# Kernel optimization log

Hardware: AMD Instinct MI355X
Metric: run time of the kernel (lower is better)

## Reference

```python
import jax, jax.numpy as jnp
import numpy as np

D = 128          # fine voxel grid resolution
N0 = 250000
D_IN, D_BASE, D_OUT = 16, 8, 8
EPS = 1e-5
# (cin, cout) for conv0..conv6, conv7, conv9, conv11
_CH = [(16, 8), (8, 16), (16, 16), (16, 32), (32, 32), (32, 64), (64, 64), (64, 32), (32, 16), (16, 8)]

def _offsets():
    r = np.arange(-1, 2)
    return np.stack(np.meshgrid(r, r, r, indexing='ij'), -1).reshape(-1, 3)  # [27,3]

def _lookup_fn(coords, d):
    keys = (coords[:, 0].astype(np.int64) * d + coords[:, 1]) * d + coords[:, 2]
    order = np.argsort(keys)
    skeys = keys[order]
    def lookup(q):
        valid = ((q >= 0) & (q < d)).all(-1)
        k = (q[:, 0].astype(np.int64) * d + q[:, 1]) * d + q[:, 2]
        pos = np.clip(np.searchsorted(skeys, k), 0, len(skeys) - 1)
        return np.where(valid & (skeys[pos] == k), order[pos], -1).astype(np.int32)
    return lookup

def _nbr_same(coords, d):
    # stride-1 sparse conv: outputs at input coords, neighbors at coord+k
    lk = _lookup_fn(coords, d)
    return np.stack([lk(coords + o) for o in _offsets()], 1)  # [N,27]

def _nbr_down(c_out, c_in, d_in):
    # stride-2 conv: output p gathers inputs at 2p+k
    lk = _lookup_fn(c_in, d_in)
    return np.stack([lk(c_out * 2 + o) for o in _offsets()], 1)

def _nbr_up(c_out, c_in, d_in):
    # transposed stride-2 conv: output q gathers input p=(q-k)/2 where divisible
    lk = _lookup_fn(c_in, d_in)
    cols = []
    for o in _offsets():
        q = c_out - o
        div = (q % 2 == 0).all(-1)
        cols.append(np.where(div, lk(q // 2), -1).astype(np.int32))
    return np.stack(cols, 1)

def setup_inputs():
    rng = np.random.default_rng(0)
    flat = rng.choice(D ** 3, size=N0, replace=False)
    c0 = np.stack([flat // (D * D), (flat // D) % D, flat % D], 1).astype(np.int32)
    c1 = np.unique(c0 // 2, axis=0)
    c2 = np.unique(c1 // 2, axis=0)
    c3 = np.unique(c2 // 2, axis=0)
    inp = {
        'feats': jax.random.normal(jax.random.key(0), (N0, D_IN), jnp.float32),
        'nbr0': jnp.asarray(_nbr_same(c0, D)),
        'nbr_d01': jnp.asarray(_nbr_down(c1, c0, D)),
        'nbr1': jnp.asarray(_nbr_same(c1, D // 2)),
        'nbr_d12': jnp.asarray(_nbr_down(c2, c1, D // 2)),
        'nbr2': jnp.asarray(_nbr_same(c2, D // 4)),
        'nbr_d23': jnp.asarray(_nbr_down(c3, c2, D // 4)),
        'nbr3': jnp.asarray(_nbr_same(c3, D // 8)),
        'nbr_u32': jnp.asarray(_nbr_up(c2, c3, D // 8)),
        'nbr_u21': jnp.asarray(_nbr_up(c1, c2, D // 4)),
        'nbr_u10': jnp.asarray(_nbr_up(c0, c1, D // 2)),
    }
    key = jax.random.key(1)
    for i, (ci, co) in enumerate(_CH):
        key, kw = jax.random.split(key)
        inp['w%d' % i] = jax.random.normal(kw, (27, ci, co), jnp.float32) / np.sqrt(27.0 * ci)
        inp['g%d' % i] = jnp.ones((co,), jnp.float32)
        inp['b%d' % i] = jnp.zeros((co,), jnp.float32)
    inp['lin_w'] = jax.random.normal(jax.random.key(2), (D_OUT, D_BASE), jnp.float32) / np.sqrt(D_BASE)
    return inp

def _sconv_bn_relu(f, nbr, w, g, b):
    # f: [Nin,Cin], nbr: [Nout,27] (-1 = no neighbor), w: [27,Cin,Cout]
    gth = jnp.where((nbr >= 0)[..., None], f[jnp.maximum(nbr, 0)], 0.0)  # [Nout,27,Cin]
    y = jnp.einsum('nkc,kco->no', gth, w)
    mu = y.mean(0)                       # training-mode BatchNorm over active voxels
    var = y.var(0)
    return jax.nn.relu((y - mu) * jax.lax.rsqrt(var + EPS) * g + b)

def reference(feats, nbr0, nbr_d01, nbr1, nbr_d12, nbr2, nbr_d23, nbr3, nbr_u32, nbr_u21, nbr_u10,
              w0, g0, b0, w1, g1, b1, w2, g2, b2, w3, g3, b3, w4, g4, b4,
              w5, g5, b5, w6, g6, b6, w7, g7, b7, w8, g8, b8, w9, g9, b9, lin_w):
    c0f = _sconv_bn_relu(feats, nbr0, w0, g0, b0)
    c2f = _sconv_bn_relu(_sconv_bn_relu(c0f, nbr_d01, w1, g1, b1), nbr1, w2, g2, b2)
    c4f = _sconv_bn_relu(_sconv_bn_relu(c2f, nbr_d12, w3, g3, b3), nbr2, w4, g4, b4)
    x = _sconv_bn_relu(_sconv_bn_relu(c4f, nbr_d23, w5, g5, b5), nbr3, w6, g6, b6)
    x = c4f + _sconv_bn_relu(x, nbr_u32, w7, g7, b7)
    x = c2f + _sconv_bn_relu(x, nbr_u21, w8, g8, b8)
    x = c0f + _sconv_bn_relu(x, nbr_u10, w9, g9, b9)
    return x @ lin_w.T, x
```

## Files before the change

kernel.cpp:

```cpp
#include <hip/hip_runtime.h>

#define EPSV 1e-5f

typedef __attribute__((ext_vector_type(8))) short short8;
typedef __attribute__((ext_vector_type(4))) float float4v;

static inline int cdiv(int a, int b) { return (a + b - 1) / b; }

__device__ inline unsigned short f2bf(float x) {
  unsigned u = __float_as_uint(x);
  return (unsigned short)((u + 0x7FFFu + ((u >> 16) & 1u)) >> 16);
}
__device__ inline float bf2f(unsigned short u) {
  return __uint_as_float(((unsigned)u) << 16);
}

#define NBUCKET 64

struct PrepArgs {
  const float* w[10];
  unsigned short* wt[10];
  int ci[10];
  int co[10];
  int wcum[11];
  const float* feats;
  unsigned short* featsb;
  int nfeat4;
  float* stats;
};

__global__ __launch_bounds__(256) void prep_kernel(PrepArgs p) {
  long tid = (long)blockIdx.x * 256 + threadIdx.x;
  const int nstat4 = 10 * NBUCKET * 128 / 4;
  if (tid < nstat4) {
    ((float4*)p.stats)[tid] = make_float4(0.f, 0.f, 0.f, 0.f);
    return;
  }
  tid -= nstat4;
  if (tid < p.nfeat4) {
    float4 v = ((const float4*)p.feats)[tid];
    ushort4 r;
    r.x = f2bf(v.x); r.y = f2bf(v.y); r.z = f2bf(v.z); r.w = f2bf(v.w);
    ((ushort4*)p.featsb)[tid] = r;
    return;
  }
  tid -= p.nfeat4;
  if (tid >= p.wcum[10]) return;
  int i = 0;
  while (tid >= p.wcum[i + 1]) ++i;
  int e = (int)(tid - p.wcum[i]);
  int ci = p.ci[i], co = p.co[i];
  int k = e / (ci * co);
  int r = e - k * (ci * co);
  int o = r / ci;
  int c = r - o * ci;
  p.wt[i][((long)k * co + o) * ci + c] = f2bf(p.w[i][((long)k * ci + c) * co + o]);
}

template<int CI, int CO>
__global__ __launch_bounds__(256) void conv_mfma(
    const unsigned short* __restrict__ f, const int* __restrict__ nbr,
    const unsigned short* __restrict__ wt, unsigned short* __restrict__ y,
    float* __restrict__ stats, int nout, int nxb) {
  constexpr int NCHUNK = (CI == 8) ? 7 : (CI == 16) ? 14 : (CI == 32) ? 27 : 54;

  int bx = blockIdx.x, xb;
  {
    int S8 = nxb >> 3;
    if (bx < (S8 << 3)) xb = (bx & 7) * S8 + (bx >> 3);
    else xb = bx;
  }

  const int tid = threadIdx.x;
  const int lane = tid & 63;
  const int wid = tid >> 6;
  const int m = lane & 15;
  const int quad = lane >> 4;
  const int blockrow = xb * 64;
  const int row = blockrow + wid * 16 + m;
  const bool rok = row < nout;
  const int cbase = blockIdx.y * 16;
  const int co = cbase + m;
  const bool cok = co < CO;

  auto tapof = [&](int c) -> int {
    if constexpr (CI == 8) return c * 4 + quad;
    else if constexpr (CI == 16) return c * 2 + (quad >> 1);
    else if constexpr (CI == 32) return c;
    else return c >> 1;
  };
  auto cioof = [&](int c) -> int {
    if constexpr (CI == 8) return 0;
    else if constexpr (CI == 16) return (quad & 1) * 8;
    else if constexpr (CI == 32) return quad * 8;
    else return ((c & 1) << 5) + quad * 8;
  };

  float4v acc = {0.f, 0.f, 0.f, 0.f};

  if constexpr (CI <= 16) {
    int idxs[NCHUNK];
#pragma unroll
    for (int c = 0; c < NCHUNK; ++c) {
      int tap = tapof(c);
      idxs[c] = (rok && tap < 27) ? nbr[(long)row * 27 + tap] : -1;
    }
    short8 A[NCHUNK], B[NCHUNK];
#pragma unroll
    for (int c = 0; c < NCHUNK; ++c) {
      int tap = tapof(c);
      short8 a, bq;
#pragma unroll
      for (int q = 0; q < 8; ++q) { a[q] = 0; bq[q] = 0; }
      if (idxs[c] >= 0) a = *(const short8*)(f + (long)idxs[c] * CI + cioof(c));
      if (cok && tap < 27) bq = *(const short8*)(wt + ((long)tap * CO + co) * CI + cioof(c));
      A[c] = a; B[c] = bq;
    }
#pragma unroll
    for (int c = 0; c < NCHUNK; ++c)
      acc = __builtin_amdgcn_mfma_f32_16x16x32_bf16(A[c], B[c], acc, 0, 0, 0);
  } else {
    constexpr int G = 9;
    constexpr int NG = NCHUNK / G;
    int idxs[27];
#pragma unroll
    for (int t = 0; t < 27; ++t)
      idxs[t] = rok ? nbr[(long)row * 27 + t] : -1;

    short8 A[2][G], B[2][G];
    auto load_group = [&](int g, int bi) {
#pragma unroll
      for (int j = 0; j < G; ++j) {
        const int c = g * G + j;
        const int tap = tapof(c);
        short8 a, bq;
#pragma unroll
        for (int q = 0; q < 8; ++q) { a[q] = 0; bq[q] = 0; }
        int idx = idxs[tap];
        if (idx >= 0) a = *(const short8*)(f + (long)idx * CI + cioof(c));
        if (cok) bq = *(const short8*)(wt + ((long)tap * CO + co) * CI + cioof(c));
        A[bi][j] = a; B[bi][j] = bq;
      }
    };
    load_group(0, 0);
#pragma unroll
    for (int g = 0; g < NG; ++g) {
      const int cur = g & 1;
      if (g + 1 < NG) load_group(g + 1, cur ^ 1);
#pragma unroll
      for (int j = 0; j < G; ++j)
        acc = __builtin_amdgcn_mfma_f32_16x16x32_bf16(A[cur][j], B[cur][j], acc, 0, 0, 0);
    }
  }

  float sum = 0.f, sq = 0.f;
#pragma unroll
  for (int r = 0; r < 4; ++r) {
    float v = acc[r];
    int orow = blockrow + wid * 16 + quad * 4 + r;
    if (cok && orow < nout) y[(long)orow * CO + co] = f2bf(v);
    sum += v;
    sq = fmaf(v, v, sq);
  }
  sum += __shfl_xor(sum, 16); sq += __shfl_xor(sq, 16);
  sum += __shfl_xor(sum, 32); sq += __shfl_xor(sq, 32);
  if (quad == 0 && cok) {
    float* st = stats + (((unsigned)xb & (NBUCKET - 1)) << 7);
    atomicAdd(&st[co], sum);
    atomicAdd(&st[64 + co], sq);
  }
}

template<int CO>
__global__ __launch_bounds__(256) void bn_relu_bf16(
    const unsigned short* __restrict__ y, const float* __restrict__ stats,
    const float* __restrict__ g, const float* __restrict__ b,
    const unsigned short* __restrict__ skip, unsigned short* __restrict__ out,
    int nout, float inv_n) {
  __shared__ float sA[CO], sC[CO];
  if ((int)threadIdx.x < CO) {
    int o = threadIdx.x;
    float su = 0.f, sq = 0.f;
#pragma unroll 8
    for (int bk = 0; bk < NBUCKET; ++bk) {
      su += stats[bk * 128 + o];
      sq += stats[bk * 128 + 64 + o];
    }
    float mu = su * inv_n;
    float var = sq * inv_n - mu * mu;
    float a = g[o] * rsqrtf(var + EPSV);
    sA[o] = a;
    sC[o] = fmaf(-mu, a, b[o]);
  }
  __syncthreads();
  long i4 = (long)blockIdx.x * 256 + threadIdx.x;
  long total4 = (long)nout * CO / 4;
  if (i4 >= total4) return;
  int o = (int)((i4 * 4) % CO);
  ushort4 v = ((const ushort4*)y)[i4];
  float vv[4] = {bf2f(v.x), bf2f(v.y), bf2f(v.z), bf2f(v.w)};
  unsigned short rr[4];
#pragma unroll
  for (int j = 0; j < 4; ++j) {
    float x = fmaxf(fmaf(vv[j], sA[o + j], sC[o + j]), 0.f);
    if (skip) x += bf2f(skip[i4 * 4 + j]);
    rr[j] = f2bf(x);
  }
  ushort4 r;
  r.x = rr[0]; r.y = rr[1]; r.z = rr[2]; r.w = rr[3];
  ((ushort4*)out)[i4] = r;
}

__global__ __launch_bounds__(256) void tail_kernel(
    const unsigned short* __restrict__ c0f, const float* __restrict__ st9,
    const float* __restrict__ g9, const float* __restrict__ b9, float inv_n,
    const float* __restrict__ lin_w, const unsigned short* __restrict__ y9,
    float* __restrict__ out0, float* __restrict__ x0, int n0) {
  __shared__ float swl[64];
  __shared__ float sbn[16];
  if (threadIdx.x < 64) swl[threadIdx.x] = lin_w[threadIdx.x];
  if (threadIdx.x < 8) {
    int o = threadIdx.x;
    float su = 0.f, sq = 0.f;
#pragma unroll 8
    for (int bk = 0; bk < NBUCKET; ++bk) {
      su += st9[bk * 128 + o];
      sq += st9[bk * 128 + 64 + o];
    }
    float mu = su * inv_n;
    float var = sq * inv_n - mu * mu;
    float a = g9[o] * rsqrtf(var + EPSV);
    sbn[o] = a;
    sbn[8 + o] = fmaf(-mu, a, b9[o]);
  }
  __syncthreads();
  int n = blockIdx.x * 256 + threadIdx.x;
  if (n >= n0) return;
  const ushort4* pr = (const ushort4*)(y9 + (long)n * 8);
  ushort4 r0 = pr[0], r1 = pr[1];
  unsigned short rw[8] = {r0.x, r0.y, r0.z, r0.w, r1.x, r1.y, r1.z, r1.w};
  const ushort4* pc = (const ushort4*)(c0f + (long)n * 8);
  ushort4 c0 = pc[0], c1 = pc[1];
  unsigned short cs[8] = {c0.x, c0.y, c0.z, c0.w, c1.x, c1.y, c1.z, c1.w};
  float xv[8];
#pragma unroll
  for (int c = 0; c < 8; ++c)
    xv[c] = bf2f(cs[c]) + fmaxf(fmaf(bf2f(rw[c]), sbn[c], sbn[8 + c]), 0.f);
  *(float4*)(x0 + (long)n * 8) = make_float4(xv[0], xv[1], xv[2], xv[3]);
  *(float4*)(x0 + (long)n * 8 + 4) = make_float4(xv[4], xv[5], xv[6], xv[7]);
  float ov[8];
#pragma unroll
  for (int j = 0; j < 8; ++j) {
    float s = 0.f;
#pragma unroll
    for (int c = 0; c < 8; ++c) s = fmaf(xv[c], swl[j * 8 + c], s);
    ov[j] = s;
  }
  *(float4*)(out0 + (long)n * 8) = make_float4(ov[0], ov[1], ov[2], ov[3]);
  *(float4*)(out0 + (long)n * 8 + 4) = make_float4(ov[4], ov[5], ov[6], ov[7]);
}

extern "C" void kernel_launch(void* const* d_in, const int* in_sizes, int n_in,
                              void* d_out, int out_size, void* d_ws, size_t ws_size,
                              hipStream_t stream) {
  const float* feats   = (const float*)d_in[0];
  const int* nbr0      = (const int*)d_in[1];
  const int* nbr_d01   = (const int*)d_in[2];
  const int* nbr1      = (const int*)d_in[3];
  const int* nbr_d12   = (const int*)d_in[4];
  const int* nbr2      = (const int*)d_in[5];
  const int* nbr_d23   = (const int*)d_in[6];
  const int* nbr3      = (const int*)d_in[7];
  const int* nbr_u32   = (const int*)d_in[8];
  const int* nbr_u21   = (const int*)d_in[9];
  const int* nbr_u10   = (const int*)d_in[10];
  const float* w[10];
  const float* g[10];
  const float* b[10];
  for (int i = 0; i < 10; ++i) {
    w[i] = (const float*)d_in[11 + 3 * i];
    g[i] = (const float*)d_in[12 + 3 * i];
    b[i] = (const float*)d_in[13 + 3 * i];
  }
  const float* lin_w = (const float*)d_in[41];

  const int N0 = in_sizes[0] / 16;
  const int N1 = in_sizes[2] / 27;
  const int N2 = in_sizes[4] / 27;
  const int N3 = in_sizes[6] / 27;
  const float i0 = 1.f / N0, i1 = 1.f / N1, i2 = 1.f / N2, i3 = 1.f / N3;

  static const int CIv[10] = {16, 8, 16, 16, 32, 32, 64, 64, 32, 16};
  static const int COv[10] = {8, 16, 16, 32, 32, 64, 64, 32, 16, 8};

  float* stats = (float*)d_ws;
  unsigned short* u = (unsigned short*)(stats + 10 * NBUCKET * 128);

  unsigned short* yraw = u; u += (size_t)N1 * 32;

  unsigned short* wt[10];
  int wcum[11];
  wcum[0] = 0;
  for (int i = 0; i < 10; ++i) {
    wt[i] = u;
    int sz = 27 * CIv[i] * COv[i];
    u += sz;
    wcum[i + 1] = wcum[i] + sz;
  }
  unsigned short* featsb = u; u += (size_t)N0 * 16;
  unsigned short* c0f = u;    u += (size_t)N0 * 8;
  unsigned short* t1  = u;    u += (size_t)N1 * 16;
  unsigned short* c2f = u;    u += (size_t)N1 * 16;
  unsigned short* t2  = u;    u += (size_t)N2 * 32;
  unsigned short* c4f = u;    u += (size_t)N2 * 32;
  unsigned short* t3  = u;    u += (size_t)N3 * 64;
  unsigned short* t4  = u;    u += (size_t)N3 * 64;
  unsigned short* t5  = t2;
  unsigned short* t6  = t1;
  float* out0 = (float*)d_out;
  float* x0   = (float*)d_out + (size_t)N0 * 8;

  float* s[10];
  for (int i = 0; i < 10; ++i) s[i] = stats + i * NBUCKET * 128;

  PrepArgs pa;
  for (int i = 0; i < 10; ++i) {
    pa.w[i] = w[i]; pa.wt[i] = wt[i];
    pa.ci[i] = CIv[i]; pa.co[i] = COv[i];
    pa.wcum[i] = wcum[i];
  }
  pa.wcum[10] = wcum[10];
  pa.feats = feats; pa.featsb = featsb;
  pa.nfeat4 = N0 * 16 / 4;
  pa.stats = stats;
  long prep_total = (10 * NBUCKET * 128 / 4) + pa.nfeat4 + wcum[10];
  prep_kernel<<<(int)((prep_total + 255) / 256), 256, 0, stream>>>(pa);

  auto bgrid = [](long nout, int co) { return (int)((nout * co / 4 + 255) / 256); };

  int xb0 = cdiv(N0, 64), xb1 = cdiv(N1, 64), xb2 = cdiv(N2, 64), xb3 = cdiv(N3, 64);

  conv_mfma<16, 8><<<dim3(xb0, 1), 256, 0, stream>>>(featsb, nbr0, wt[0], yraw, s[0], N0, xb0);
  bn_relu_bf16<8><<<bgrid(N0, 8), 256, 0, stream>>>(yraw, s[0], g[0], b[0], nullptr, c0f, N0, i0);

  conv_mfma<8, 16><<<dim3(xb1, 1), 256, 0, stream>>>(c0f, nbr_d01, wt[1], yraw, s[1], N1, xb1);
  bn_relu_bf16<16><<<bgrid(N1, 16), 256, 0, stream>>>(yraw, s[1], g[1], b[1], nullptr, t1, N1, i1);

  conv_mfma<16, 16><<<dim3(xb1, 1), 256, 0, stream>>>(t1, nbr1, wt[2], yraw, s[2], N1, xb1);
  bn_relu_bf16<16><<<bgrid(N1, 16), 256, 0, stream>>>(yraw, s[2], g[2], b[2], nullptr, c2f, N1, i1);

  conv_mfma<16, 32><<<dim3(xb2, 2), 256, 0, stream>>>(c2f, nbr_d12, wt[3], yraw, s[3], N2, xb2);
  bn_relu_bf16<32><<<bgrid(N2, 32), 256, 0, stream>>>(yraw, s[3], g[3], b[3], nullptr, t2, N2, i2);

  conv_mfma<32, 32><<<dim3(xb2, 2), 256, 0, stream>>>(t2, nbr2, wt[4], yraw, s[4], N2, xb2);
  bn_relu_bf16<32><<<bgrid(N2, 32), 256, 0, stream>>>(yraw, s[4], g[4], b[4], nullptr, c4f, N2, i2);

  conv_mfma<32, 64><<<dim3(xb3, 4), 256, 0, stream>>>(c4f, nbr_d23, wt[5], yraw, s[5], N3, xb3);
  bn_relu_bf16<64><<<bgrid(N3, 64), 256, 0, stream>>>(yraw, s[5], g[5], b[5], nullptr, t3, N3, i3);

  conv_mfma<64, 64><<<dim3(xb3, 4), 256, 0, stream>>>(t3, nbr3, wt[6], yraw, s[6], N3, xb3);
  bn_relu_bf16<64><<<bgrid(N3, 64), 256, 0, stream>>>(yraw, s[6], g[6], b[6], nullptr, t4, N3, i3);

  conv_mfma<64, 32><<<dim3(xb2, 2), 256, 0, stream>>>(t4, nbr_u32, wt[7], yraw, s[7], N2, xb2);
  bn_relu_bf16<32><<<bgrid(N2, 32), 256, 0, stream>>>(yraw, s[7], g[7], b[7], c4f, t5, N2, i2);

  conv_mfma<32, 16><<<dim3(xb1, 1), 256, 0, stream>>>(t5, nbr_u21, wt[8], yraw, s[8], N1, xb1);
  bn_relu_bf16<16><<<bgrid(N1, 16), 256, 0, stream>>>(yraw, s[8], g[8], b[8], c2f, t6, N1, i1);

  conv_mfma<16, 8><<<dim3(xb0, 1), 256, 0, stream>>>(t6, nbr_u10, wt[9], yraw, s[9], N0, xb0);

  tail_kernel<<<cdiv(N0, 256), 256, 0, stream>>>(c0f, s[9], g[9], b[9], i0, lin_w, yraw, out0, x0, N0);
}
```

Baseline: 501.8 us.

## Convert conv and elementwise kernels to grid-stride persistent loops

Every kernel (prep, conv, BN-ReLU, tail) now runs a grid-stride loop, with grids capped at 1024 or 2048 blocks. For the small-CI convs the weight fragments are loaded once per block and reused across tiles, and BN stat partial sums accumulate in registers across tiles, so fewer atomics are issued. The XCD-aware block swizzle is dropped, and stat buckets are now keyed by block and wave. The cost is less latency hiding from oversubscription and possible load imbalance, since consecutive tiles no longer map to the same XCD.

New measurement: 480.0 us. 1.05x faster.

```diff
diff --git a/kernel.cpp b/kernel.cpp
--- a/kernel.cpp
+++ b/kernel.cpp
@@ -6,6 +6,7 @@
 typedef __attribute__((ext_vector_type(4))) float float4v;
 
 static inline int cdiv(int a, int b) { return (a + b - 1) / b; }
+static inline int imin(int a, int b) { return a < b ? a : b; }
 
 __device__ inline unsigned short f2bf(float x) {
   unsigned u = __float_as_uint(x);
@@ -29,56 +30,49 @@
   float* stats;
 };
 
-__global__ __launch_bounds__(256) void prep_kernel(PrepArgs p) {
-  long tid = (long)blockIdx.x * 256 + threadIdx.x;
+__global__ __launch_bounds__(256) void prep_kernel(PrepArgs p, long total) {
   const int nstat4 = 10 * NBUCKET * 128 / 4;
-  if (tid < nstat4) {
-    ((float4*)p.stats)[tid] = make_float4(0.f, 0.f, 0.f, 0.f);
-    return;
-  }
-  tid -= nstat4;
-  if (tid < p.nfeat4) {
-    float4 v = ((const float4*)p.feats)[tid];
-    ushort4 r;
-    r.x = f2bf(v.x); r.y = f2bf(v.y); r.z = f2bf(v.z); r.w = f2bf(v.w);
-    ((ushort4*)p.featsb)[tid] = r;
-    return;
-  }
-  tid -= p.nfeat4;
-  if (tid >= p.wcum[10]) return;
-  int i = 0;
-  while (tid >= p.wcum[i + 1]) ++i;
-  int e = (int)(tid - p.wcum[i]);
-  int ci = p.ci[i], co = p.co[i];
-  int k = e / (ci * co);
-  int r = e - k * (ci * co);
-  int o = r / ci;
-  int c = r - o * ci;
-  p.wt[i][((long)k * co + o) * ci + c] = f2bf(p.w[i][((long)k * ci + c) * co + o]);
+  for (long tid0 = (long)blockIdx.x * 256 + threadIdx.x; tid0 < total;
+       tid0 += (long)gridDim.x * 256) {
+    long tid = tid0;
+    if (tid < nstat4) {
+      ((float4*)p.stats)[tid] = make_float4(0.f, 0.f, 0.f, 0.f);
+      continue;
+    }
+    tid -= nstat4;
+    if (tid < p.nfeat4) {
+      float4 v = ((const float4*)p.feats)[tid];
+      ushort4 r;
+      r.x = f2bf(v.x); r.y = f2bf(v.y); r.z = f2bf(v.z); r.w = f2bf(v.w);
+      ((ushort4*)p.featsb)[tid] = r;
+      continue;
+    }
+    tid -= p.nfeat4;
+    if (tid >= p.wcum[10]) continue;
+    int i = 0;
+    while (tid >= p.wcum[i + 1]) ++i;
+    int e = (int)(tid - p.wcum[i]);
+    int ci = p.ci[i], co = p.co[i];
+    int k = e / (ci * co);
+    int r = e - k * (ci * co);
+    int o = r / ci;
+    int c = r - o * ci;
+    p.wt[i][((long)k * co + o) * ci + c] = f2bf(p.w[i][((long)k * ci + c) * co + o]);
+  }
 }
 
 template<int CI, int CO>
 __global__ __launch_bounds__(256) void conv_mfma(
     const unsigned short* __restrict__ f, const int* __restrict__ nbr,
     const unsigned short* __restrict__ wt, unsigned short* __restrict__ y,
-    float* __restrict__ stats, int nout, int nxb) {
+    float* __restrict__ stats, int nout, int ntiles) {
   constexpr int NCHUNK = (CI == 8) ? 7 : (CI == 16) ? 14 : (CI == 32) ? 27 : 54;
-
-  int bx = blockIdx.x, xb;
-  {
-    int S8 = nxb >> 3;
-    if (bx < (S8 << 3)) xb = (bx & 7) * S8 + (bx >> 3);
-    else xb = bx;
-  }
 
   const int tid = threadIdx.x;
   const int lane = tid & 63;
   const int wid = tid >> 6;
   const int m = lane & 15;
   const int quad = lane >> 4;
-  const int blockrow = xb * 64;
-  const int row = blockrow + wid * 16 + m;
-  const bool rok = row < nout;
   const int cbase = blockIdx.y * 16;
   const int co = cbase + m;
   const bool cok = co < CO;
@@ -96,76 +90,103 @@
     else return ((c & 1) << 5) + quad * 8;
   };
 
-  float4v acc = {0.f, 0.f, 0.f, 0.f};
+  float sum = 0.f, sq = 0.f;
 
   if constexpr (CI <= 16) {
-    int idxs[NCHUNK];
+    short8 Bv[NCHUNK];
 #pragma unroll
     for (int c = 0; c < NCHUNK; ++c) {
       int tap = tapof(c);
-      idxs[c] = (rok && tap < 27) ? nbr[(long)row * 27 + tap] : -1;
-    }
-    short8 A[NCHUNK], B[NCHUNK];
-#pragma unroll
-    for (int c = 0; c < NCHUNK; ++c) {
-      int tap = tapof(c);
-      short8 a, bq;
-#pragma unroll
-      for (int q = 0; q < 8; ++q) { a[q] = 0; bq[q] = 0; }
-      if (idxs[c] >= 0) a = *(const short8*)(f + (long)idxs[c] * CI + cioof(c));
+      short8 bq;
+#pragma unroll
+      for (int q = 0; q < 8; ++q) bq[q] = 0;
       if (cok && tap < 27) bq = *(const short8*)(wt + ((long)tap * CO + co) * CI + cioof(c));
-      A[c] = a; B[c] = bq;
-    }
-#pragma unroll
-    for (int c = 0; c < NCHUNK; ++c)
-      acc = __builtin_amdgcn_mfma_f32_16x16x32_bf16(A[c], B[c], acc, 0, 0, 0);
+      Bv[c] = bq;
+    }
+    for (int tile = blockIdx.x; tile < ntiles; tile += gridDim.x) {
+      const int rowb = tile * 64 + wid * 16;
+      const int row = rowb + m;
+      const bool rok = row < nout;
+      int idxs[NCHUNK];
+#pragma unroll
+      for (int c = 0; c < NCHUNK; ++c) {
+        int tap = tapof(c);
+        idxs[c] = (rok && tap < 27) ? nbr[(long)row * 27 + tap] : -1;
+      }
+      short8 A[NCHUNK];
+#pragma unroll
+      for (int c = 0; c < NCHUNK; ++c) {
+        short8 a;
+#pragma unroll
+        for (int q = 0; q < 8; ++q) a[q] = 0;
+        if (idxs[c] >= 0) a = *(const short8*)(f + (long)idxs[c] * CI + cioof(c));
+        A[c] = a;
+      }
+      float4v acc = {0.f, 0.f, 0.f, 0.f};
+#pragma unroll
+      for (int c = 0; c < NCHUNK; ++c)
+        acc = __builtin_amdgcn_mfma_f32_16x16x32_bf16(A[c], Bv[c], acc, 0, 0, 0);
+#pragma unroll
+      for (int r = 0; r < 4; ++r) {
+        float v = acc[r];
+        int orow = rowb + quad * 4 + r;
+        if (cok && orow < nout) y[(long)orow * CO + co] = f2bf(v);
+        sum += v;
+        sq = fmaf(v, v, sq);
+      }
+    }
   } else {
     constexpr int G = 9;
     constexpr int NG = NCHUNK / G;
-    int idxs[27];
-#pragma unroll
-    for (int t = 0; t < 27; ++t)
-      idxs[t] = rok ? nbr[(long)row * 27 + t] : -1;
-
-    short8 A[2][G], B[2][G];
-    auto load_group = [&](int g, int bi) {
-#pragma unroll
-      for (int j = 0; j < G; ++j) {
-        const int c = g * G + j;
-        const int tap = tapof(c);
-        short8 a, bq;
-#pragma unroll
-        for (int q = 0; q < 8; ++q) { a[q] = 0; bq[q] = 0; }
-        int idx = idxs[tap];
-        if (idx >= 0) a = *(const short8*)(f + (long)idx * CI + cioof(c));
-        if (cok) bq = *(const short8*)(wt + ((long)tap * CO + co) * CI + cioof(c));
-        A[bi][j] = a; B[bi][j] = bq;
-      }
-    };
-    load_group(0, 0);
-#pragma unroll
-    for (int g = 0; g < NG; ++g) {
-      const int cur = g & 1;
-      if (g + 1 < NG) load_group(g + 1, cur ^ 1);
-#pragma unroll
-      for (int j = 0; j < G; ++j)
-        acc = __builtin_amdgcn_mfma_f32_16x16x32_bf16(A[cur][j], B[cur][j], acc, 0, 0, 0);
-    }
-  }
-
-  float sum = 0.f, sq = 0.f;
-#pragma unroll
-  for (int r = 0; r < 4; ++r) {
-    float v = acc[r];
-    int orow = blockrow + wid * 16 + quad * 4 + r;
-    if (cok && orow < nout) y[(long)orow * CO + co] = f2bf(v);
-    sum += v;
-    sq = fmaf(v, v, sq);
-  }
+    for (int tile = blockIdx.x; tile < ntiles; tile += gridDim.x) {
+      const int rowb = tile * 64 + wid * 16;
+      const int row = rowb + m;
+      const bool rok = row < nout;
+      int idxs[27];
+#pragma unroll
+      for (int t = 0; t < 27; ++t)
+        idxs[t] = rok ? nbr[(long)row * 27 + t] : -1;
+
+      short8 A[2][G], B[2][G];
+      auto load_group = [&](int g, int bi) {
+#pragma unroll
+        for (int j = 0; j < G; ++j) {
+          const int c = g * G + j;
+          const int tap = tapof(c);
+          short8 a, bq;
+#pragma unroll
+          for (int q = 0; q < 8; ++q) { a[q] = 0; bq[q] = 0; }
+          int idx = idxs[tap];
+          if (idx >= 0) a = *(const short8*)(f + (long)idx * CI + cioof(c));
+          if (cok) bq = *(const short8*)(wt + ((long)tap * CO + co) * CI + cioof(c));
+          A[bi][j] = a; B[bi][j] = bq;
+        }
+      };
+      float4v acc = {0.f, 0.f, 0.f, 0.f};
+      load_group(0, 0);
+#pragma unroll
+      for (int g = 0; g < NG; ++g) {
+        const int cur = g & 1;
+        if (g + 1 < NG) load_group(g + 1, cur ^ 1);
+#pragma unroll
+        for (int j = 0; j < G; ++j)
+          acc = __builtin_amdgcn_mfma_f32_16x16x32_bf16(A[cur][j], B[cur][j], acc, 0, 0, 0);
+      }
+#pragma unroll
+      for (int r = 0; r < 4; ++r) {
+        float v = acc[r];
+        int orow = rowb + quad * 4 + r;
+        if (cok && orow < nout) y[(long)orow * CO + co] = f2bf(v);
+        sum += v;
+        sq = fmaf(v, v, sq);
+      }
+    }
+  }
+
   sum += __shfl_xor(sum, 16); sq += __shfl_xor(sq, 16);
   sum += __shfl_xor(sum, 32); sq += __shfl_xor(sq, 32);
   if (quad == 0 && cok) {
-    float* st = stats + (((unsigned)xb & (NBUCKET - 1)) << 7);
+    float* st = stats + ((((unsigned)blockIdx.x * 4 + wid) & (NBUCKET - 1)) << 7);
     atomicAdd(&st[co], sum);
     atomicAdd(&st[64 + co], sq);
   }
@@ -193,22 +214,23 @@
     sC[o] = fmaf(-mu, a, b[o]);
   }
   __syncthreads();
-  long i4 = (long)blockIdx.x * 256 + threadIdx.x;
   long total4 = (long)nout * CO / 4;
-  if (i4 >= total4) return;
-  int o = (int)((i4 * 4) % CO);
-  ushort4 v = ((const ushort4*)y)[i4];
-  float vv[4] = {bf2f(v.x), bf2f(v.y), bf2f(v.z), bf2f(v.w)};
-  unsigned short rr[4];
-#pragma unroll
-  for (int j = 0; j < 4; ++j) {
-    float x = fmaxf(fmaf(vv[j], sA[o + j], sC[o + j]), 0.f);
-    if (skip) x += bf2f(skip[i4 * 4 + j]);
-    rr[j] = f2bf(x);
-  }
-  ushort4 r;
-  r.x = rr[0]; r.y = rr[1]; r.z = rr[2]; r.w = rr[3];
-  ((ushort4*)out)[i4] = r;
+  for (long i4 = (long)blockIdx.x * 256 + threadIdx.x; i4 < total4;
+       i4 += (long)gridDim.x * 256) {
+    int o = (int)((i4 * 4) % CO);
+    ushort4 v = ((const ushort4*)y)[i4];
+    float vv[4] = {bf2f(v.x), bf2f(v.y), bf2f(v.z), bf2f(v.w)};
+    unsigned short rr[4];
+#pragma unroll
+    for (int j = 0; j < 4; ++j) {
+      float x = fmaxf(fmaf(vv[j], sA[o + j], sC[o + j]), 0.f);
+      if (skip) x += bf2f(skip[i4 * 4 + j]);
+      rr[j] = f2bf(x);
+    }
+    ushort4 r;
+    r.x = rr[0]; r.y = rr[1]; r.z = rr[2]; r.w = rr[3];
+    ((ushort4*)out)[i4] = r;
+  }
 }
 
 __global__ __launch_bounds__(256) void tail_kernel(
@@ -234,30 +256,30 @@
     sbn[8 + o] = fmaf(-mu, a, b9[o]);
   }
   __syncthreads();
-  int n = blockIdx.x * 256 + threadIdx.x;
-  if (n >= n0) return;
-  const ushort4* pr = (const ushort4*)(y9 + (long)n * 8);
-  ushort4 r0 = pr[0], r1 = pr[1];
-  unsigned short rw[8] = {r0.x, r0.y, r0.z, r0.w, r1.x, r1.y, r1.z, r1.w};
-  const ushort4* pc = (const ushort4*)(c0f + (long)n * 8);
-  ushort4 c0 = pc[0], c1 = pc[1];
-  unsigned short cs[8] = {c0.x, c0.y, c0.z, c0.w, c1.x, c1.y, c1.z, c1.w};
-  float xv[8];
-#pragma unroll
-  for (int c = 0; c < 8; ++c)
-    xv[c] = bf2f(cs[c]) + fmaxf(fmaf(bf2f(rw[c]), sbn[c], sbn[8 + c]), 0.f);
-  *(float4*)(x0 + (long)n * 8) = make_float4(xv[0], xv[1], xv[2], xv[3]);
-  *(float4*)(x0 + (long)n * 8 + 4) = make_float4(xv[4], xv[5], xv[6], xv[7]);
-  float ov[8];
-#pragma unroll
-  for (int j = 0; j < 8; ++j) {
-    float s = 0.f;
-#pragma unroll
-    for (int c = 0; c < 8; ++c) s = fmaf(xv[c], swl[j * 8 + c], s);
-    ov[j] = s;
-  }
-  *(float4*)(out0 + (long)n * 8) = make_float4(ov[0], ov[1], ov[2], ov[3]);
-  *(float4*)(out0 + (long)n * 8 + 4) = make_float4(ov[4], ov[5], ov[6], ov[7]);
+  for (int n = blockIdx.x * 256 + threadIdx.x; n < n0; n += gridDim.x * 256) {
+    const ushort4* pr = (const ushort4*)(y9 + (long)n * 8);
+    ushort4 r0 = pr[0], r1 = pr[1];
+    unsigned short rw[8] = {r0.x, r0.y, r0.z, r0.w, r1.x, r1.y, r1.z, r1.w};
+    const ushort4* pc = (const ushort4*)(c0f + (long)n * 8);
+    ushort4 c0 = pc[0], c1 = pc[1];
+    unsigned short cs[8] = {c0.x, c0.y, c0.z, c0.w, c1.x, c1.y, c1.z, c1.w};
+    float xv[8];
+#pragma unroll
+    for (int c = 0; c < 8; ++c)
+      xv[c] = bf2f(cs[c]) + fmaxf(fmaf(bf2f(rw[c]), sbn[c], sbn[8 + c]), 0.f);
+    *(float4*)(x0 + (long)n * 8) = make_float4(xv[0], xv[1], xv[2], xv[3]);
+    *(float4*)(x0 + (long)n * 8 + 4) = make_float4(xv[4], xv[5], xv[6], xv[7]);
+    float ov[8];
+#pragma unroll
+    for (int j = 0; j < 8; ++j) {
+      float s = 0.f;
+#pragma unroll
+      for (int c = 0; c < 8; ++c) s = fmaf(xv[c], swl[j * 8 + c], s);
+      ov[j] = s;
+    }
+    *(float4*)(out0 + (long)n * 8) = make_float4(ov[0], ov[1], ov[2], ov[3]);
+    *(float4*)(out0 + (long)n * 8 + 4) = make_float4(ov[4], ov[5], ov[6], ov[7]);
+  }
 }
 
 extern "C" void kernel_launch(void* const* d_in, const int* in_sizes, int n_in,
@@ -334,40 +356,44 @@
   pa.nfeat4 = N0 * 16 / 4;
   pa.stats = stats;
   long prep_total = (10 * NBUCKET * 128 / 4) + pa.nfeat4 + wcum[10];
-  prep_kernel<<<(int)((prep_total + 255) / 256), 256, 0, stream>>>(pa);
-
-  auto bgrid = [](long nout, int co) { return (int)((nout * co / 4 + 255) / 256); };
-
-  int xb0 = cdiv(N0, 64), xb1 = cdiv(N1, 64), xb2 = cdiv(N2, 64), xb3 = cdiv(N3, 64);
-
-  conv_mfma<16, 8><<<dim3(xb0, 1), 256, 0, stream>>>(featsb, nbr0, wt[0], yraw, s[0], N0, xb0);
+  prep_kernel<<<imin((int)((prep_total + 255) / 256), 2048), 256, 0, stream>>>(pa, prep_total);
+
+  auto bgrid = [](long nout, int co) {
+    return imin((int)((nout * co / 4 + 255) / 256), 1024);
+  };
+  auto cgrid = [](int ntiles) { return imin(ntiles, 1024); };
+
+  int tb0 = cdiv(N0, 64), tb1 = cdiv(N1, 64), tb2 = cdiv(N2, 64), tb3 = cdiv(N3, 64);
+
+  conv_mfma<16, 8><<<dim3(cgrid(tb0), 1), 256, 0, stream>>>(featsb, nbr0, wt[0], yraw, s[0], N0, tb0);
   bn_relu_bf16<8><<<bgrid(N0, 8), 256, 0, stream>>>(yraw, s[0], g[0], b[0], nullptr, c0f, N0, i0);
 
-  conv_mfma<8, 16><<<dim3(xb1, 1), 256, 0, stream>>>(c0f, nbr_d01, wt[1], yraw, s[1], N1, xb1);
+  conv_mfma<8, 16><<<dim3(cgrid(tb1), 1), 256, 0, stream>>>(c0f, nbr_d01, wt[1], yraw, s[1], N1, tb1);
   bn_relu_bf16<16><<<bgrid(N1, 16), 256, 0, stream>>>(yraw, s[1], g[1], b[1], nullptr, t1, N1, i1);
 
-  conv_mfma<16, 16><<<dim3(xb1, 1), 256, 0, stream>>>(t1, nbr1, wt[2], yraw, s[2], N1, xb1);
+  conv_mfma<16, 16><<<dim3(cgrid(tb1), 1), 256, 0, stream>>>(t1, nbr1, wt[2], yraw, s[2], N1, tb1);
   bn_relu_bf16<16><<<bgrid(N1, 16), 256, 0, stream>>>(yraw, s[2], g[2], b[2], nullptr, c2f, N1, i1);
 
-  conv_mfma<16, 32><<<dim3(xb2, 2), 256, 0, stream>>>(c2f, nbr_d12, wt[3], yraw, s[3], N2, xb2);
+  conv_mfma<16, 32><<<dim3(cgrid(tb2), 2), 256, 0, stream>>>(c2f, nbr_d12, wt[3], yraw, s[3], N2, tb2);
   bn_relu_bf16<32><<<bgrid(N2, 32), 256, 0, stream>>>(yraw, s[3], g[3], b[3], nullptr, t2, N2, i2);
 
-  conv_mfma<32, 32><<<dim3(xb2, 2), 256, 0, stream>>>(t2, nbr2, wt[4], yraw, s[4], N2, xb2);
+  conv_mfma<32, 32><<<dim3(cgrid(tb2), 2), 256, 0, stream>>>(t2, nbr2, wt[4], yraw, s[4], N2, tb2);
   bn_relu_bf16<32><<<bgrid(N2, 32), 256, 0, stream>>>(yraw, s[4], g[4], b[4], nullptr, c4f, N2, i2);
 
-  conv_mfma<32, 64><<<dim3(xb3, 4), 256, 0, stream>>>(c4f, nbr_d23, wt[5], yraw, s[5], N3, xb3);
+  conv_mfma<32, 64><<<dim3(cgrid(tb3), 4), 256, 0, stream>>>(c4f, nbr_d23, wt[5], yraw, s[5], N3, tb3);
   bn_relu_bf16<64><<<bgrid(N3, 64), 256, 0, stream>>>(yraw, s[5], g[5], b[5], nullptr, t3, N3, i3);
 
-  conv_mfma<64, 64><<<dim3(xb3, 4), 256, 0, stream>>>(t3, nbr3, wt[6], yraw, s[6], N3, xb3);
+  conv_mfma<64, 64><<<dim3(cgrid(tb3), 4), 256, 0, stream>>>(t3, nbr3, wt[6], yraw, s[6], N3, tb3);
   bn_relu_bf16<64><<<bgrid(N3, 64), 256, 0, stream>>>(yraw, s[6], g[6], b[6], nullptr, t4, N3, i3);
 
-  conv_mfma<64, 32><<<dim3(xb2, 2), 256, 0, stream>>>(t4, nbr_u32, wt[7], yraw, s[7], N2, xb2);
+  conv_mfma<64, 32><<<dim3(cgrid(tb2), 2), 256, 0, stream>>>(t4, nbr_u32, wt[7], yraw, s[7], N2, tb2);
   bn_relu_bf16<32><<<bgrid(N2, 32), 256, 0, stream>>>(yraw, s[7], g[7], b[7], c4f, t5, N2, i2);
 
-  conv_mfma<32, 16><<<dim3(xb1, 1), 256, 0, stream>>>(t5, nbr_u21, wt[8], yraw, s[8], N1, xb1);
+  conv_mfma<32, 16><<<dim3(cgrid(tb1), 1), 256, 0, stream>>>(t5, nbr_u21, wt[8], yraw, s[8], N1, tb1);
   bn_relu_bf16<16><<<bgrid(N1, 16), 256, 0, stream>>>(yraw, s[8], g[8], b[8], c2f, t6, N1, i1);
 
-  conv_mfma<16, 8><<<dim3(xb0, 1), 256, 0, stream>>>(t6, nbr_u10, wt[9], yraw, s[9], N0, xb0);
-
-  tail_kernel<<<cdiv(N0, 256), 256, 0, stream>>>(c0f, s[9], g[9], b[9], i0, lin_w, yraw, out0, x0, N0);
-}
+  conv_mfma<16, 8><<<dim3(cgrid(tb0), 1), 256, 0, stream>>>(t6, nbr_u10, wt[9], yraw, s[9], N0, tb0);
+
+  tail_kernel<<<imin(cdiv(N0, 256), 1024), 256, 0, stream>>>(
+      c0f, s[9], g[9], b[9], i0, lin_w, yraw, out0, x0, N0);
+}
```
